# Performance work log

Measured on AMD Instinct MI355X. Metric: run time of the kernel, lower is better.

Reference implementation:

```python
import jax, jax.numpy as jnp
import numpy as np
from jax import lax

BIG = 1e10  # initial 'infinite' distance, matching torch's 1e10


def farthest_point_sample(xyz, npoint):
    # xyz: [B, N, 3] float; returns centroids: [B, npoint] int32
    B, N, _ = xyz.shape

    def step(carry, _):
        distance, farthest = carry            # [B,N], [B]
        # gather current farthest point per batch -> [B,1,3]
        centroid = jnp.take_along_axis(xyz, farthest[:, None, None], axis=1)
        dist = jnp.sum((xyz - centroid) ** 2, axis=-1)   # [B,N]
        distance = jnp.minimum(distance, dist)           # running min distance
        new_farthest = jnp.argmax(distance, axis=-1).astype(jnp.int32)
        # emit the index selected at THIS iteration (torch stores before update)
        return (distance, new_farthest), farthest

    init = (jnp.full((B, N), BIG, dtype=xyz.dtype),
            jnp.zeros((B,), dtype=jnp.int32))
    _, centroids = lax.scan(step, init, None, length=npoint)  # [npoint, B]
    return centroids.T  # [B, npoint]


def setup_inputs() -> dict:
    key = jax.random.key(0)
    B, N = 8, 131072
    xyz = jax.random.normal(key, (B, N, 3), dtype=jnp.float32)
    return {"xyz": xyz, "points": 1024}


def reference(xyz, points):
    return farthest_point_sample(xyz, points)
```

## Files before the change

### kernel.cpp

```cpp
#include <hip/hip_runtime.h>
#include <stdint.h>


#define NPTS        131072
#define NBATCH      8
#define WGB         32
#define THREADS     256
#define PPW         4096
#define SLOT_STRIDE 16
#define BIGDIST     1e10f

typedef unsigned long long u64;

__global__ __launch_bounds__(THREADS, 1) void fps_kernel(
        const float* __restrict__ xyz,
        int* __restrict__ out,
        u64* __restrict__ ws,
        int npoint)
{
    const int bid  = blockIdx.x;
    const int b    = bid & (NBATCH - 1);
    const int w    = bid >> 3;
    const int tid  = threadIdx.x;
    const int lane = tid & 63;
    const int v    = tid >> 6;

    const float* base = xyz + (size_t)b * NPTS * 3;
    const int q0 = w * PPW;

    __shared__ __align__(16) float x_lds[PPW];
    __shared__ __align__(16) float y_lds[PPW];
    __shared__ __align__(16) float z_lds[PPW];
    __shared__ u64   s_w[THREADS / 64];
    __shared__ float s_c[3];
    __shared__ int   s_f;
    __shared__ int   s_fast;

    #pragma unroll
    for (int j = 0; j < 16; ++j) {
        int q = tid + 256 * j;
        const float* p = base + (size_t)(q0 + q) * 3;
        x_lds[q] = p[0];
        y_lds[q] = p[1];
        z_lds[q] = p[2];
    }

    u64* slots  = ws;
    u64* census = ws + (size_t)2 * NBATCH * WGB * SLOT_STRIDE;

    if (v == 0) {
        unsigned xcc;
        asm volatile("s_getreg_b32 %0, hwreg(HW_REG_XCC_ID)" : "=s"(xcc));
        u64* cb = census + (size_t)b * WGB * SLOT_STRIDE;
        if (lane == 0) {
            __hip_atomic_store(cb + (size_t)w * SLOT_STRIDE,
                               (0xC0DEC0DEull << 32) | (u64)xcc,
                               __ATOMIC_RELAXED, __HIP_MEMORY_SCOPE_AGENT);
        }
        u64 cv = 0;
        if (lane < WGB) {
            u64* cl = cb + (size_t)lane * SLOT_STRIDE;
            do {
                cv = __hip_atomic_load(cl, __ATOMIC_RELAXED,
                                       __HIP_MEMORY_SCOPE_AGENT);
            } while ((cv >> 32) != 0xC0DEC0DEull);
        }
        unsigned my = (unsigned)cv;
        unsigned x0 = __shfl(my, 0);
        bool same = (lane >= WGB) || (my == x0);
        if (lane == 0) s_fast = (__ballot(same) == ~0ull) ? 1 : 0;
    }

    float dist[16];
    #pragma unroll
    for (int j = 0; j < 16; ++j) dist[j] = BIGDIST;

    float cx = base[0], cy = base[1], cz = base[2];
    if (w == 0 && tid == 0) out[b * npoint + 0] = 0;

    __syncthreads();
    const int fast = s_fast;

    const size_t PAR = (size_t)NBATCH * WGB * SLOT_STRIDE;
    u64* sbase = slots + (size_t)b * WGB * SLOT_STRIDE;

    for (int i = 0; i < npoint - 1; ++i) {
        float bv = -1.0f; int bq = 0;
        {
            #pragma clang fp contract(off)
            #pragma unroll
            for (int g = 0; g < 4; ++g) {
                const int qg = 4 * tid + 1024 * g;
                float4 xv = *reinterpret_cast<const float4*>(&x_lds[qg]);
                float4 yv = *reinterpret_cast<const float4*>(&y_lds[qg]);
                float4 zv = *reinterpret_cast<const float4*>(&z_lds[qg]);
                float xs[4] = { xv.x, xv.y, xv.z, xv.w };
                float ys[4] = { yv.x, yv.y, yv.z, yv.w };
                float zs[4] = { zv.x, zv.y, zv.z, zv.w };
                #pragma unroll
                for (int e = 0; e < 4; ++e) {
                    const int j = 4 * g + e;
                    float dx = xs[e] - cx, dy = ys[e] - cy, dz = zs[e] - cz;
                    float d  = dx*dx + dy*dy + dz*dz;
                    float nd = fminf(dist[j], d);
                    dist[j]  = nd;
                    if (nd > bv) { bv = nd; bq = qg + e; }
                }
            }
        }
        u64 pk = ((u64)__float_as_uint(bv) << 32)
               | (u64)(0x1FFFFu - (unsigned)(q0 + bq));

        #pragma unroll
        for (int m = 32; m >= 1; m >>= 1) {
            u64 o = __shfl_xor(pk, m);
            if (o > pk) pk = o;
        }
        if (lane == 0) s_w[v] = pk;
        __syncthreads();

        u64* sb = sbase + ((i & 1) ? PAR : (size_t)0);
        const unsigned tag = (unsigned)(i + 1);

        if (v == 0) {
            u64 c = s_w[lane & 3];
            u64 o1 = __shfl_xor(c, 1); if (o1 > c) c = o1;
            u64 o2 = __shfl_xor(c, 2); if (o2 > c) c = o2;

            if (lane == 0) {
                u64 pub = c | ((u64)tag << 22);
                u64* my = sb + (size_t)w * SLOT_STRIDE;
                if (fast) {
                    __hip_atomic_exchange(my, pub, __ATOMIC_RELAXED,
                                          __HIP_MEMORY_SCOPE_WORKGROUP);
                } else {
                    __hip_atomic_store(my, pub, __ATOMIC_RELAXED,
                                       __HIP_MEMORY_SCOPE_AGENT);
                }
            }

            u64 s = 0;
            if (lane < WGB) {
                u64* sl = sb + (size_t)lane * SLOT_STRIDE;
                if (fast) {
                    do {
                        s = __hip_atomic_fetch_or(sl, 0ull, __ATOMIC_RELAXED,
                                                  __HIP_MEMORY_SCOPE_WORKGROUP);
                    } while (((unsigned)(s >> 22) & 1023u) != tag);
                } else {
                    do {
                        s = __hip_atomic_load(sl, __ATOMIC_RELAXED,
                                              __HIP_MEMORY_SCOPE_AGENT);
                    } while (((unsigned)(s >> 22) & 1023u) != tag);
                }
            }
            int idx_l = (int)(0x1FFFFu - (unsigned)(s & 0x1FFFFu));
            float ccx = 0.f, ccy = 0.f, ccz = 0.f;
            if (lane < WGB) {
                const float* cp = base + (size_t)idx_l * 3;
                ccx = cp[0]; ccy = cp[1]; ccz = cp[2];
            }
            u64 mx = s;
            #pragma unroll
            for (int m = 32; m >= 1; m >>= 1) {
                u64 o = __shfl_xor(mx, m);
                if (o > mx) mx = o;
            }
            u64 ball = __ballot(lane < WGB && s == mx);
            int winlane = __ffsll(ball) - 1;
            float wx = __shfl(ccx, winlane);
            float wy = __shfl(ccy, winlane);
            float wz = __shfl(ccz, winlane);
            int  wix = __shfl(idx_l, winlane);
            if (lane == 0) {
                s_c[0] = wx; s_c[1] = wy; s_c[2] = wz; s_f = wix;
                if (w == 0) out[b * npoint + (i + 1)] = wix;
            }
        }
        __syncthreads();

        cx = s_c[0]; cy = s_c[1]; cz = s_c[2];
    }
}

extern "C" void kernel_launch(void* const* d_in, const int* in_sizes, int n_in,
                              void* d_out, int out_size, void* d_ws, size_t ws_size,
                              hipStream_t stream) {
    const float* xyz = (const float*)d_in[0];
    int* out = (int*)d_out;
    u64* ws = (u64*)d_ws;
    const int npoint = out_size / NBATCH;

    hipMemsetAsync(d_ws, 0,
                   (size_t)(2 * NBATCH * WGB + NBATCH * WGB) * SLOT_STRIDE * sizeof(u64),
                   stream);

    dim3 grid(NBATCH * WGB);
    dim3 block(THREADS);
    fps_kernel<<<grid, block, 0, stream>>>(xyz, out, ws, npoint);
}
```

Before: 2.384 ms.

## Remap batches to XCCs and publish winner coordinates with slot tags

Workgroups now count themselves per XCC at startup. When the 256 workgroups split evenly into 32 per XCC, each batch is assigned to a single XCC, so the workgroup-scope atomics stay within one L2. Each workgroup also publishes its candidate's xyz coordinates in tagged slot words. The reader can then take the winning centroid from the exchanged data, which removes the dependent global load of the coordinates after the reduction. Polling uses paired 64-bit atomic ORs in inline asm across all 64 lanes. This adds more atomic traffic per iteration and relies on tag-ordering assumptions across separate slot words.

```diff
diff --git a/kernel.cpp b/kernel.cpp
--- a/kernel.cpp
+++ b/kernel.cpp
@@ -8,33 +8,88 @@
 #define THREADS     256
 #define PPW         4096
 #define SLOT_STRIDE 16
+#define NWG         (NBATCH * WGB)
 #define BIGDIST     1e10f
 
 typedef unsigned long long u64;
+
+static __device__ __forceinline__ void wg_swap(u64* p, u64 v) {
+    asm volatile("global_atomic_swap_x2 %0, %1, off"
+                 :: "v"(p), "v"(v) : "memory");
+}
+static __device__ __forceinline__ void wg_or2(u64* p, u64& a, u64& b) {
+    u64 z = 0;
+    asm volatile("global_atomic_or_x2 %0, %2, %4, off sc0\n\t"
+                 "global_atomic_or_x2 %1, %3, %4, off sc0\n\t"
+                 "s_waitcnt vmcnt(0)"
+                 : "=&v"(a), "=&v"(b)
+                 : "v"(p), "v"(p + 1), "v"(z)
+                 : "memory");
+}
 
 __global__ __launch_bounds__(THREADS, 1) void fps_kernel(
         const float* __restrict__ xyz,
         int* __restrict__ out,
-        u64* __restrict__ ws,
+        u64* __restrict__ wsbuf,
         int npoint)
 {
     const int bid  = blockIdx.x;
-    const int b    = bid & (NBATCH - 1);
-    const int w    = bid >> 3;
     const int tid  = threadIdx.x;
     const int lane = tid & 63;
     const int v    = tid >> 6;
 
-    const float* base = xyz + (size_t)b * NPTS * 3;
-    const int q0 = w * PPW;
+    u64* slots  = wsbuf;
+    u64* census = wsbuf + (size_t)2 * NBATCH * WGB * SLOT_STRIDE;
+    u64* cnt    = census + (size_t)NWG * SLOT_STRIDE;
 
     __shared__ __align__(16) float x_lds[PPW];
     __shared__ __align__(16) float y_lds[PPW];
     __shared__ __align__(16) float z_lds[PPW];
     __shared__ u64   s_w[THREADS / 64];
     __shared__ float s_c[3];
-    __shared__ int   s_f;
-    __shared__ int   s_fast;
+    __shared__ int   s_role;
+
+    if (v == 0) {
+        unsigned myxcc = 0, myord = 0;
+        if (lane == 0) {
+            asm volatile("s_getreg_b32 %0, hwreg(HW_REG_XCC_ID)" : "=s"(myxcc));
+            myord = (unsigned)__hip_atomic_fetch_add(
+                        cnt + (size_t)(myxcc & 7) * SLOT_STRIDE, 1ull,
+                        __ATOMIC_RELAXED, __HIP_MEMORY_SCOPE_AGENT);
+            __hip_atomic_store(census + (size_t)bid * SLOT_STRIDE,
+                               (0xC0DEC0DEull << 32) |
+                                   ((u64)(myxcc & 255u) << 8) | (u64)(myord & 255u),
+                               __ATOMIC_RELAXED, __HIP_MEMORY_SCOPE_AGENT);
+        }
+        bool okr = true; u64 acc = 0;
+        #pragma unroll
+        for (int k = 0; k < 4; ++k) {
+            u64* ce = census + (size_t)(lane + 64 * k) * SLOT_STRIDE;
+            u64 c;
+            do {
+                c = __hip_atomic_load(ce, __ATOMIC_RELAXED,
+                                      __HIP_MEMORY_SCOPE_AGENT);
+            } while ((c >> 32) != 0xC0DEC0DEull);
+            unsigned xc = (unsigned)((c >> 8) & 255u);
+            okr = okr && (xc < 8u);
+            acc += 1ull << (8 * (xc & 7u));
+        }
+        #pragma unroll
+        for (int m = 1; m <= 32; m <<= 1) acc += __shfl_xor(acc, m);
+        bool balanced = (acc == 0x2020202020202020ull) &&
+                        (__ballot(okr) == ~0ull);
+        if (lane == 0)
+            s_role = balanced ? ((1 << 16) | (int)((myxcc & 7u) << 8) | (int)myord)
+                              : 0;
+    }
+    __syncthreads();
+
+    const int fast = (s_role >> 16) & 1;
+    const int b    = fast ? ((s_role >> 8) & 255) : (bid & 7);
+    const int w    = fast ? (s_role & 255)        : (bid >> 3);
+
+    const float* base = xyz + (size_t)b * NPTS * 3;
+    const int q0 = w * PPW;
 
     #pragma unroll
     for (int j = 0; j < 16; ++j) {
@@ -45,32 +100,6 @@
         z_lds[q] = p[2];
     }
 
-    u64* slots  = ws;
-    u64* census = ws + (size_t)2 * NBATCH * WGB * SLOT_STRIDE;
-
-    if (v == 0) {
-        unsigned xcc;
-        asm volatile("s_getreg_b32 %0, hwreg(HW_REG_XCC_ID)" : "=s"(xcc));
-        u64* cb = census + (size_t)b * WGB * SLOT_STRIDE;
-        if (lane == 0) {
-            __hip_atomic_store(cb + (size_t)w * SLOT_STRIDE,
-                               (0xC0DEC0DEull << 32) | (u64)xcc,
-                               __ATOMIC_RELAXED, __HIP_MEMORY_SCOPE_AGENT);
-        }
-        u64 cv = 0;
-        if (lane < WGB) {
-            u64* cl = cb + (size_t)lane * SLOT_STRIDE;
-            do {
-                cv = __hip_atomic_load(cl, __ATOMIC_RELAXED,
-                                       __HIP_MEMORY_SCOPE_AGENT);
-            } while ((cv >> 32) != 0xC0DEC0DEull);
-        }
-        unsigned my = (unsigned)cv;
-        unsigned x0 = __shfl(my, 0);
-        bool same = (lane >= WGB) || (my == x0);
-        if (lane == 0) s_fast = (__ballot(same) == ~0ull) ? 1 : 0;
-    }
-
     float dist[16];
     #pragma unroll
     for (int j = 0; j < 16; ++j) dist[j] = BIGDIST;
@@ -79,7 +108,6 @@
     if (w == 0 && tid == 0) out[b * npoint + 0] = 0;
 
     __syncthreads();
-    const int fast = s_fast;
 
     const size_t PAR = (size_t)NBATCH * WGB * SLOT_STRIDE;
     u64* sbase = slots + (size_t)b * WGB * SLOT_STRIDE;
@@ -128,53 +156,71 @@
             u64 o2 = __shfl_xor(c, 2); if (o2 > c) c = o2;
 
             if (lane == 0) {
-                u64 pub = c | ((u64)tag << 22);
+                int idx_wg = (int)(0x1FFFFu - (unsigned)(c & 0x1FFFFu));
+                int qw = idx_wg - q0;
+                u64 tw = ((u64)tag << 32);
+                u64 w1 = tw | (u64)__float_as_uint(x_lds[qw]);
+                u64 w2 = tw | (u64)__float_as_uint(y_lds[qw]);
+                u64 w3 = tw | (u64)__float_as_uint(z_lds[qw]);
+                u64 w0 = c | ((u64)tag << 22);
                 u64* my = sb + (size_t)w * SLOT_STRIDE;
                 if (fast) {
-                    __hip_atomic_exchange(my, pub, __ATOMIC_RELAXED,
-                                          __HIP_MEMORY_SCOPE_WORKGROUP);
+                    wg_swap(my + 1, w1); wg_swap(my + 2, w2);
+                    wg_swap(my + 3, w3); wg_swap(my + 0, w0);
                 } else {
-                    __hip_atomic_store(my, pub, __ATOMIC_RELAXED,
-                                       __HIP_MEMORY_SCOPE_AGENT);
+                    __hip_atomic_store(my + 1, w1, __ATOMIC_RELAXED, __HIP_MEMORY_SCOPE_AGENT);
+                    __hip_atomic_store(my + 2, w2, __ATOMIC_RELAXED, __HIP_MEMORY_SCOPE_AGENT);
+                    __hip_atomic_store(my + 3, w3, __ATOMIC_RELAXED, __HIP_MEMORY_SCOPE_AGENT);
+                    __hip_atomic_store(my + 0, w0, __ATOMIC_RELAXED, __HIP_MEMORY_SCOPE_AGENT);
                 }
             }
 
-            u64 s = 0;
-            if (lane < WGB) {
-                u64* sl = sb + (size_t)lane * SLOT_STRIDE;
-                if (fast) {
-                    do {
-                        s = __hip_atomic_fetch_or(sl, 0ull, __ATOMIC_RELAXED,
-                                                  __HIP_MEMORY_SCOPE_WORKGROUP);
-                    } while (((unsigned)(s >> 22) & 1023u) != tag);
-                } else {
-                    do {
-                        s = __hip_atomic_load(sl, __ATOMIC_RELAXED,
-                                              __HIP_MEMORY_SCOPE_AGENT);
-                    } while (((unsigned)(s >> 22) & 1023u) != tag);
-                }
-            }
-            int idx_l = (int)(0x1FFFFu - (unsigned)(s & 0x1FFFFu));
-            float ccx = 0.f, ccy = 0.f, ccz = 0.f;
-            if (lane < WGB) {
-                const float* cp = base + (size_t)idx_l * 3;
-                ccx = cp[0]; ccy = cp[1]; ccz = cp[2];
-            }
-            u64 mx = s;
+            const int  s    = lane >> 1;
+            const bool even = (lane & 1) == 0;
+            u64* sp = sb + (size_t)s * SLOT_STRIDE + (even ? 0 : 2);
+            u64 wa = 0, wb = 0;
+            bool oka = false, okb = false;
+            if (fast) {
+                do {
+                    wg_or2(sp, wa, wb);
+                    oka = (even ? (unsigned)((wa >> 22) & 1023u)
+                                : (unsigned)((wa >> 32) & 1023u)) == tag;
+                    okb = ((unsigned)((wb >> 32) & 1023u) == tag);
+                } while (__ballot(oka && okb) != ~0ull);
+            } else {
+                do {
+                    if (!oka) {
+                        wa = __hip_atomic_load(sp + 0, __ATOMIC_RELAXED,
+                                               __HIP_MEMORY_SCOPE_AGENT);
+                        oka = (even ? (unsigned)((wa >> 22) & 1023u)
+                                    : (unsigned)((wa >> 32) & 1023u)) == tag;
+                    }
+                    if (!okb) {
+                        wb = __hip_atomic_load(sp + 1, __ATOMIC_RELAXED,
+                                               __HIP_MEMORY_SCOPE_AGENT);
+                        okb = ((unsigned)((wb >> 32) & 1023u) == tag);
+                    }
+                } while (__ballot(oka && okb) != ~0ull);
+            }
+
+            u64 mx = even ? wa : 0;
             #pragma unroll
             for (int m = 32; m >= 1; m >>= 1) {
                 u64 o = __shfl_xor(mx, m);
                 if (o > mx) mx = o;
             }
-            u64 ball = __ballot(lane < WGB && s == mx);
-            int winlane = __ffsll(ball) - 1;
-            float wx = __shfl(ccx, winlane);
-            float wy = __shfl(ccy, winlane);
-            float wz = __shfl(ccz, winlane);
-            int  wix = __shfl(idx_l, winlane);
+            int idx_win = (int)(0x1FFFFu - (unsigned)(mx & 0x1FFFFu));
+            int sw = idx_win >> 12;
+
+            float fxx = even ? __uint_as_float((unsigned)wb) : 0.f;
+            float fyy = even ? 0.f : __uint_as_float((unsigned)wa);
+            float fzz = even ? 0.f : __uint_as_float((unsigned)wb);
+            float nx = __shfl(fxx, 2 * sw);
+            float ny = __shfl(fyy, 2 * sw + 1);
+            float nz = __shfl(fzz, 2 * sw + 1);
             if (lane == 0) {
-                s_c[0] = wx; s_c[1] = wy; s_c[2] = wz; s_f = wix;
-                if (w == 0) out[b * npoint + (i + 1)] = wix;
+                s_c[0] = nx; s_c[1] = ny; s_c[2] = nz;
+                if (w == 0) out[b * npoint + (i + 1)] = idx_win;
             }
         }
         __syncthreads();
@@ -188,14 +234,14 @@
                               hipStream_t stream) {
     const float* xyz = (const float*)d_in[0];
     int* out = (int*)d_out;
-    u64* ws = (u64*)d_ws;
+    u64* wsbuf = (u64*)d_ws;
     const int npoint = out_size / NBATCH;
 
     hipMemsetAsync(d_ws, 0,
-                   (size_t)(2 * NBATCH * WGB + NBATCH * WGB) * SLOT_STRIDE * sizeof(u64),
+                   (size_t)(2 * NBATCH * WGB + NWG + NBATCH) * SLOT_STRIDE * sizeof(u64),
                    stream);
 
-    dim3 grid(NBATCH * WGB);
+    dim3 grid(NWG);
     dim3 block(THREADS);
-    fps_kernel<<<grid, block, 0, stream>>>(xyz, out, ws, npoint);
-}
+    fps_kernel<<<grid, block, 0, stream>>>(xyz, out, wsbuf, npoint);
+}
```

Result: slower. 3.218 ms (+35.0%).

## Replace workgroup barriers with tagged LDS flags and drop XCC census fast path

Applied to the files above, without the earlier changes.

Removes both __syncthreads per iteration. Wave leaders now publish tagged partial maxima into LDS, wave 0 spins on those tags, and wave 0 broadcasts the new centroid through tagged LDS words that the other waves poll with s_sleep. The XCC census and its workgroup-scope atomic fast path are also dropped, so every cross-block exchange now uses agent-scope store and load. This aims to cut barrier latency on the serial critical path, but the busy-polling waves compete for issue slots and losing the fast path may make global exchange slower.

```diff
diff --git a/kernel.cpp b/kernel.cpp
--- a/kernel.cpp
+++ b/kernel.cpp
@@ -15,7 +15,7 @@
 __global__ __launch_bounds__(THREADS, 1) void fps_kernel(
         const float* __restrict__ xyz,
         int* __restrict__ out,
-        u64* __restrict__ ws,
+        u64* __restrict__ slots,
         int npoint)
 {
     const int bid  = blockIdx.x;
@@ -31,10 +31,8 @@
     __shared__ __align__(16) float x_lds[PPW];
     __shared__ __align__(16) float y_lds[PPW];
     __shared__ __align__(16) float z_lds[PPW];
-    __shared__ u64   s_w[THREADS / 64];
-    __shared__ float s_c[3];
-    __shared__ int   s_f;
-    __shared__ int   s_fast;
+    __shared__ u64 s_w[4];
+    __shared__ u64 s_cw[3];
 
     #pragma unroll
     for (int j = 0; j < 16; ++j) {
@@ -44,32 +42,8 @@
         y_lds[q] = p[1];
         z_lds[q] = p[2];
     }
-
-    u64* slots  = ws;
-    u64* census = ws + (size_t)2 * NBATCH * WGB * SLOT_STRIDE;
-
-    if (v == 0) {
-        unsigned xcc;
-        asm volatile("s_getreg_b32 %0, hwreg(HW_REG_XCC_ID)" : "=s"(xcc));
-        u64* cb = census + (size_t)b * WGB * SLOT_STRIDE;
-        if (lane == 0) {
-            __hip_atomic_store(cb + (size_t)w * SLOT_STRIDE,
-                               (0xC0DEC0DEull << 32) | (u64)xcc,
-                               __ATOMIC_RELAXED, __HIP_MEMORY_SCOPE_AGENT);
-        }
-        u64 cv = 0;
-        if (lane < WGB) {
-            u64* cl = cb + (size_t)lane * SLOT_STRIDE;
-            do {
-                cv = __hip_atomic_load(cl, __ATOMIC_RELAXED,
-                                       __HIP_MEMORY_SCOPE_AGENT);
-            } while ((cv >> 32) != 0xC0DEC0DEull);
-        }
-        unsigned my = (unsigned)cv;
-        unsigned x0 = __shfl(my, 0);
-        bool same = (lane >= WGB) || (my == x0);
-        if (lane == 0) s_fast = (__ballot(same) == ~0ull) ? 1 : 0;
-    }
+    if (tid < 4) s_w[tid] = 0;
+    if (tid < 3) s_cw[tid] = 0;
 
     float dist[16];
     #pragma unroll
@@ -79,7 +53,6 @@
     if (w == 0 && tid == 0) out[b * npoint + 0] = 0;
 
     __syncthreads();
-    const int fast = s_fast;
 
     const size_t PAR = (size_t)NBATCH * WGB * SLOT_STRIDE;
     u64* sbase = slots + (size_t)b * WGB * SLOT_STRIDE;
@@ -108,7 +81,9 @@
                 }
             }
         }
+        const unsigned tag = (unsigned)(i + 1);
         u64 pk = ((u64)__float_as_uint(bv) << 32)
+               | ((u64)tag << 22)
                | (u64)(0x1FFFFu - (unsigned)(q0 + bq));
 
         #pragma unroll
@@ -116,43 +91,34 @@
             u64 o = __shfl_xor(pk, m);
             if (o > pk) pk = o;
         }
-        if (lane == 0) s_w[v] = pk;
-        __syncthreads();
+        if (lane == 0)
+            __hip_atomic_store(&s_w[v], pk, __ATOMIC_RELAXED,
+                               __HIP_MEMORY_SCOPE_WORKGROUP);
 
         u64* sb = sbase + ((i & 1) ? PAR : (size_t)0);
-        const unsigned tag = (unsigned)(i + 1);
 
         if (v == 0) {
-            u64 c = s_w[lane & 3];
+            u64 c = 0;
+            if (lane < 4) {
+                do {
+                    c = __hip_atomic_load(&s_w[lane], __ATOMIC_RELAXED,
+                                          __HIP_MEMORY_SCOPE_WORKGROUP);
+                } while (((unsigned)(c >> 22) & 1023u) != tag);
+            }
             u64 o1 = __shfl_xor(c, 1); if (o1 > c) c = o1;
             u64 o2 = __shfl_xor(c, 2); if (o2 > c) c = o2;
 
-            if (lane == 0) {
-                u64 pub = c | ((u64)tag << 22);
-                u64* my = sb + (size_t)w * SLOT_STRIDE;
-                if (fast) {
-                    __hip_atomic_exchange(my, pub, __ATOMIC_RELAXED,
-                                          __HIP_MEMORY_SCOPE_WORKGROUP);
-                } else {
-                    __hip_atomic_store(my, pub, __ATOMIC_RELAXED,
-                                       __HIP_MEMORY_SCOPE_AGENT);
-                }
-            }
+            if (lane == 0)
+                __hip_atomic_store(sb + (size_t)w * SLOT_STRIDE, c,
+                                   __ATOMIC_RELAXED, __HIP_MEMORY_SCOPE_AGENT);
 
             u64 s = 0;
             if (lane < WGB) {
                 u64* sl = sb + (size_t)lane * SLOT_STRIDE;
-                if (fast) {
-                    do {
-                        s = __hip_atomic_fetch_or(sl, 0ull, __ATOMIC_RELAXED,
-                                                  __HIP_MEMORY_SCOPE_WORKGROUP);
-                    } while (((unsigned)(s >> 22) & 1023u) != tag);
-                } else {
-                    do {
-                        s = __hip_atomic_load(sl, __ATOMIC_RELAXED,
-                                              __HIP_MEMORY_SCOPE_AGENT);
-                    } while (((unsigned)(s >> 22) & 1023u) != tag);
-                }
+                do {
+                    s = __hip_atomic_load(sl, __ATOMIC_RELAXED,
+                                          __HIP_MEMORY_SCOPE_AGENT);
+                } while (((unsigned)(s >> 22) & 1023u) != tag);
             }
             int idx_l = (int)(0x1FFFFu - (unsigned)(s & 0x1FFFFu));
             float ccx = 0.f, ccy = 0.f, ccz = 0.f;
@@ -168,18 +134,37 @@
             }
             u64 ball = __ballot(lane < WGB && s == mx);
             int winlane = __ffsll(ball) - 1;
-            float wx = __shfl(ccx, winlane);
-            float wy = __shfl(ccy, winlane);
-            float wz = __shfl(ccz, winlane);
-            int  wix = __shfl(idx_l, winlane);
-            if (lane == 0) {
-                s_c[0] = wx; s_c[1] = wy; s_c[2] = wz; s_f = wix;
-                if (w == 0) out[b * npoint + (i + 1)] = wix;
-            }
+            cx = __shfl(ccx, winlane);
+            cy = __shfl(ccy, winlane);
+            cz = __shfl(ccz, winlane);
+            int wix = __shfl(idx_l, winlane);
+
+            float my3[3] = { cx, cy, cz };
+            if (lane < 3)
+                __hip_atomic_store(&s_cw[lane],
+                                   ((u64)tag << 32) |
+                                       (u64)__float_as_uint(my3[lane]),
+                                   __ATOMIC_RELAXED, __HIP_MEMORY_SCOPE_WORKGROUP);
+            if (w == 0 && lane == 0) out[b * npoint + (i + 1)] = wix;
+        } else {
+            u64 c0, c1, c2;
+            bool k0 = false, k1 = false, k2 = false;
+            do {
+                __builtin_amdgcn_s_sleep(1);
+                if (!k0) { c0 = __hip_atomic_load(&s_cw[0], __ATOMIC_RELAXED,
+                                   __HIP_MEMORY_SCOPE_WORKGROUP);
+                           k0 = ((unsigned)(c0 >> 32) == tag); }
+                if (!k1) { c1 = __hip_atomic_load(&s_cw[1], __ATOMIC_RELAXED,
+                                   __HIP_MEMORY_SCOPE_WORKGROUP);
+                           k1 = ((unsigned)(c1 >> 32) == tag); }
+                if (!k2) { c2 = __hip_atomic_load(&s_cw[2], __ATOMIC_RELAXED,
+                                   __HIP_MEMORY_SCOPE_WORKGROUP);
+                           k2 = ((unsigned)(c2 >> 32) == tag); }
+            } while (!(k0 && k1 && k2));
+            cx = __uint_as_float((unsigned)c0);
+            cy = __uint_as_float((unsigned)c1);
+            cz = __uint_as_float((unsigned)c2);
         }
-        __syncthreads();
-
-        cx = s_c[0]; cy = s_c[1]; cz = s_c[2];
     }
 }
 
@@ -188,14 +173,14 @@
                               hipStream_t stream) {
     const float* xyz = (const float*)d_in[0];
     int* out = (int*)d_out;
-    u64* ws = (u64*)d_ws;
+    u64* slots = (u64*)d_ws;
     const int npoint = out_size / NBATCH;
 
     hipMemsetAsync(d_ws, 0,
-                   (size_t)(2 * NBATCH * WGB + NBATCH * WGB) * SLOT_STRIDE * sizeof(u64),
+                   (size_t)2 * NBATCH * WGB * SLOT_STRIDE * sizeof(u64),
                    stream);
 
     dim3 grid(NBATCH * WGB);
     dim3 block(THREADS);
-    fps_kernel<<<grid, block, 0, stream>>>(xyz, out, ws, npoint);
+    fps_kernel<<<grid, block, 0, stream>>>(xyz, out, slots, npoint);
 }
```

Result: slower. 2.502 ms (+4.9%).
